# Performance work log

Measured on AMD Instinct MI355X. Metric: run time of the kernel, lower is better.

## Reference

```python
import jax, jax.numpy as jnp
import numpy as np
from jax import lax

B, NM, P, F, E, H, K = 32, 131072, 256, 3, 64, 4, 3
DH = E // H


def layer_norm(x, gamma, beta, eps=1e-5):
    mu = x.mean(-1, keepdims=True)
    var = ((x - mu) ** 2).mean(-1, keepdims=True)
    return (x - mu) * lax.rsqrt(var + eps) * gamma + beta


def knn_interp(x, pos_x, pos_y, k=K):
    """x: [B, Nx, F] features at pos_x [Nx, 2]; interpolate to pos_y [Ny, 2].
    Positions are shared across the batch (they are tiled in the torch code),
    so KNN indices/weights are computed once. Matches torch knn + inverse-
    squared-distance weighted scatter (uniform per-batch counts => gather form).
    """
    d2 = jnp.sum((pos_y[:, None, :] - pos_x[None, :, :]) ** 2, axis=-1)  # [Ny, Nx]
    neg_d2, idx = lax.top_k(-d2, k)                                      # [Ny, k]
    w = 1.0 / jnp.clip(-neg_d2, 1e-16)                                   # [Ny, k]
    w = lax.stop_gradient(w)  # torch computes weights under no_grad
    gathered = x[:, idx, :]                                              # [B, Ny, k, F]
    num = jnp.sum(gathered * w[None, :, :, None], axis=2)                # [B, Ny, F]
    den = jnp.sum(w, axis=1)[None, :, None]                              # [1, Ny, 1]
    return num / den


def setup_inputs() -> dict:
    key = jax.random.key(0)
    ks = jax.random.split(key, 8)
    return {
        "node_attr": jax.random.normal(ks[0], (B * NM, F), jnp.float32),
        "position_mesh": jax.random.uniform(ks[1], (NM, 2), jnp.float32),
        "position_pivotal": jax.random.uniform(ks[2], (P, 2), jnp.float32),
        "ln_gamma": jnp.ones((F,), jnp.float32),
        "ln_beta": jnp.zeros((F,), jnp.float32),
        "Wf": jax.random.normal(ks[3], (E, F), jnp.float32) * (2.0 / E) ** 0.5,
        "bf": jnp.zeros((E,), jnp.float32),
        "Wp": jax.random.normal(ks[4], (E, 2), jnp.float32) * (2.0 / E) ** 0.5,
        "bp": jnp.zeros((E,), jnp.float32),
        "in_proj_w": jax.random.normal(ks[5], (3 * E, E), jnp.float32) * (1.0 / E) ** 0.5,
        "in_proj_b": jnp.zeros((3 * E,), jnp.float32),
        "batch_size": B,
    }


def reference(node_attr, position_mesh, position_pivotal, ln_gamma, ln_beta,
              Wf, bf, Wp, bp, in_proj_w, in_proj_b, batch_size):
    x = node_attr.reshape(batch_size, -1, F)                 # [B, NM, F]
    # PivotalNorm after encoder (encoder/decoder MeshGraphNet omitted: undefined dep)
    x = layer_norm(x, ln_gamma, ln_beta)
    # ---- downsample: mesh -> pivotal via inverse-distance KNN interpolation ----
    y = knn_interp(x, position_mesh, position_pivotal)       # [B, P, F]
    # attention-based pooling over pivotal nodes
    q = (jnp.einsum('bpf,ef->bpe', y, Wf) + bf
         + (position_pivotal @ Wp.T + bp)[None])             # [B, P, E]
    Wq, Wk = in_proj_w[:E], in_proj_w[E:2 * E]
    bq, bk = in_proj_b[:E], in_proj_b[E:2 * E]
    Q = (q @ Wq.T + bq).reshape(batch_size, P, H, DH)
    Kt = (q @ Wk.T + bk).reshape(batch_size, P, H, DH)
    scores = jnp.einsum('bqhd,bkhd->bhqk', Q, Kt) / np.float32(np.sqrt(DH))
    attn = jax.nn.softmax(scores, axis=-1)                   # [B, H, P, P]
    attn_w = attn.mean(axis=1)                               # avg heads, [B, P, P]
    y = jnp.einsum('bqk,bkf->bqf', attn_w, y)                # [B, P, F]
    # ---- interpolate: pivotal -> mesh ----
    out = knn_interp(y, position_pivotal, position_mesh)     # [B, NM, F]
    return out.reshape(-1, F)
```

## Files before the change

kernel.cpp:

```cpp
#include <hip/hip_runtime.h>
#include <math.h>

#define NM 131072
#define PP 256
#define BB 32
#define INF_F 3.0e38f

#define GM   64
#define GM2  (GM * GM)
#define CAPM 96
#define GP   16
#define GP2  (GP * GP)
#define CAPP 8

typedef unsigned long long u64;

__device__ __forceinline__ u64 packkey(float d, int i) {
  return ((u64)__float_as_uint(d) << 32) | (unsigned)i;
}

__device__ __forceinline__ void ins3k(u64 k, u64& k0, u64& k1, u64& k2) {
  bool l0 = k < k0, l1 = k < k1, l2 = k < k2;
  k2 = l1 ? k1 : (l2 ? k : k2);
  k1 = l0 ? k0 : (l1 ? k : k1);
  k0 = l0 ? k : k0;
}

__device__ __forceinline__ float dist2(float ax, float ay, float bx, float by) {
  float dx = ax - bx, dy = ay - by;
  return __fadd_rn(__fmul_rn(dx, dx), __fmul_rn(dy, dy));
}

__global__ __launch_bounds__(256)
void build_buckets(const float* __restrict__ mesh, const float* __restrict__ piv,
                   unsigned* __restrict__ cntM, unsigned* __restrict__ cntP,
                   unsigned* __restrict__ ovfc,
                   float* __restrict__ bufM,
                   int* __restrict__ bufP,
                   float* __restrict__ ovfM, int* __restrict__ ovfP,
                   float* __restrict__ y2) {
  const int g = blockIdx.x * 256 + threadIdx.x;
  if (g < NM) {
    float2 mp = ((const float2*)mesh)[g];
    int cx = min((int)(mp.x * GM), GM - 1);
    int cy = min((int)(mp.y * GM), GM - 1);
    int c = cy * GM + cx;
    unsigned s = atomicAdd(&cntM[c], 1u);
    if (s < CAPM) {
      float* d = bufM + (size_t)(c * CAPM + s) * 3;
      d[0] = mp.x; d[1] = mp.y; ((int*)d)[2] = g;
    } else {
      unsigned o = atomicAdd(&ovfc[0], 1u);
      float* d = ovfM + (size_t)o * 3;
      d[0] = mp.x; d[1] = mp.y; ((int*)d)[2] = g;
    }
  }
  if (blockIdx.x == 0 && threadIdx.x < PP) {
    const int p = threadIdx.x;
    float2 pv = ((const float2*)piv)[p];
    int cx = min((int)(pv.x * GP), GP - 1);
    int cy = min((int)(pv.y * GP), GP - 1);
    int c = cy * GP + cx;
    unsigned s = atomicAdd(&cntP[c], 1u);
    if (s < CAPP) bufP[c * CAPP + s] = p;
    else { unsigned o = atomicAdd(&ovfc[1], 1u); ovfP[o] = p; }
  }
  if (blockIdx.x == 1) {
    for (int j = threadIdx.x; j < BB * PP * 4; j += 256) y2[j] = 0.f;
  }
}

__global__ __launch_bounds__(256)
void knnA_grid(const float* __restrict__ piv,
               const unsigned* __restrict__ cntM, const float* __restrict__ bufM,
               const unsigned* __restrict__ ovfc, const float* __restrict__ ovfM,
               float* __restrict__ wA, int* __restrict__ idxA) {
  const int p = blockIdx.x;
  const int t = threadIdx.x;
  __shared__ u64 sk[256 * 3];
  __shared__ u64 g3[3];
  __shared__ int sdone;

  const float2 pv = ((const float2*)piv)[p];
  const int cx = min((int)(pv.x * GM), GM - 1);
  const int cy = min((int)(pv.y * GM), GM - 1);

  u64 b0 = ~0ull, b1 = ~0ull, b2 = ~0ull;

  {
    int x0 = max(cx - 1, 0), x1 = min(cx + 1, GM - 1);
    int y0 = max(cy - 1, 0), y1 = min(cy + 1, GM - 1);
    for (int yy = y0; yy <= y1; ++yy) {
      int cb = yy * GM + x0;
      int tot = (x1 - x0 + 1) * CAPM;
      for (int s = t; s < tot; s += 256) {
        int ci = s / CAPM, j = s - ci * CAPM;
        int c = cb + ci;
        if (j < (int)min(cntM[c], (unsigned)CAPM)) {
          const float* cp = bufM + (size_t)(c * CAPM + j) * 3;
          float d = dist2(pv.x, pv.y, cp[0], cp[1]);
          ins3k(packkey(d, ((const int*)cp)[2]), b0, b1, b2);
        }
      }
    }
    int no = (int)ovfc[0];
    for (int j = t; j < no; j += 256) {
      const float* cp = ovfM + (size_t)j * 3;
      float d = dist2(pv.x, pv.y, cp[0], cp[1]);
      ins3k(packkey(d, ((const int*)cp)[2]), b0, b1, b2);
    }
  }

  int R = 1;
  u64 p0 = ~0ull, p1 = ~0ull, p2 = ~0ull;
  while (true) {
    sk[t * 3 + 0] = b0; sk[t * 3 + 1] = b1; sk[t * 3 + 2] = b2;
    __syncthreads();
    if (t < 32) {
      u64 e0 = ~0ull, e1 = ~0ull, e2 = ~0ull;
#pragma unroll
      for (int s = 0; s < 8; ++s) {
        int o = (t + 32 * s) * 3;
        ins3k(sk[o], e0, e1, e2); ins3k(sk[o + 1], e0, e1, e2); ins3k(sk[o + 2], e0, e1, e2);
      }
      sk[t * 3] = e0; sk[t * 3 + 1] = e1; sk[t * 3 + 2] = e2;
    }
    __syncthreads();
    if (t == 0) {
      u64 e0 = p0, e1 = p1, e2 = p2;
      for (int s = 0; s < 32; ++s) {
        ins3k(sk[s * 3], e0, e1, e2); ins3k(sk[s * 3 + 1], e0, e1, e2); ins3k(sk[s * 3 + 2], e0, e1, e2);
      }
      g3[0] = e0; g3[1] = e1; g3[2] = e2;
      float d2f = __uint_as_float((unsigned)(e2 >> 32));
      float md = (float)R * (1.0f / GM);
      sdone = (md * md > d2f) ? 1 : 0;
    }
    __syncthreads();
    if (sdone) break;
    p0 = g3[0]; p1 = g3[1]; p2 = g3[2];
    b0 = b1 = b2 = ~0ull;
    R += 1;
    int x0 = max(cx - R, 0), x1 = min(cx + R, GM - 1);
    for (int pass = 0; pass < 2; ++pass) {
      int yy = pass ? cy + R : cy - R;
      if (yy < 0 || yy > GM - 1) continue;
      int cb = yy * GM + x0;
      int tot = (x1 - x0 + 1) * CAPM;
      for (int s = t; s < tot; s += 256) {
        int ci = s / CAPM, j = s - ci * CAPM;
        int c = cb + ci;
        if (j < (int)min(cntM[c], (unsigned)CAPM)) {
          const float* cp = bufM + (size_t)(c * CAPM + j) * 3;
          float d = dist2(pv.x, pv.y, cp[0], cp[1]);
          ins3k(packkey(d, ((const int*)cp)[2]), b0, b1, b2);
        }
      }
    }
    int yy0 = max(cy - R + 1, 0), yy1 = min(cy + R - 1, GM - 1);
    for (int pass = 0; pass < 2; ++pass) {
      int xx = pass ? cx + R : cx - R;
      if (xx < 0 || xx > GM - 1) continue;
      int tot = (yy1 - yy0 + 1) * CAPM;
      for (int s = t; s < tot; s += 256) {
        int ri = s / CAPM, j = s - ri * CAPM;
        int c = (yy0 + ri) * GM + xx;
        if (j < (int)min(cntM[c], (unsigned)CAPM)) {
          const float* cp = bufM + (size_t)(c * CAPM + j) * 3;
          float d = dist2(pv.x, pv.y, cp[0], cp[1]);
          ins3k(packkey(d, ((const int*)cp)[2]), b0, b1, b2);
        }
      }
    }
    __syncthreads();
  }
  if (t == 0) {
#pragma unroll
    for (int k = 0; k < 3; ++k) {
      u64 e = g3[k];
      float d = __uint_as_float((unsigned)(e >> 32));
      wA[p * 3 + k] = 1.0f / fmaxf(d, 1e-16f);
      idxA[p * 3 + k] = (int)(unsigned)(e & 0xffffffffu);
    }
  }
}

__global__ __launch_bounds__(128, 2)
void gather_qqk(const float* __restrict__ node, const float* __restrict__ piv,
                const float* __restrict__ gamma, const float* __restrict__ beta,
                const float* __restrict__ Wf, const float* __restrict__ bf,
                const float* __restrict__ Wp, const float* __restrict__ bp,
                const float* __restrict__ ipw, const float* __restrict__ ipb,
                const float* __restrict__ wA, const int* __restrict__ idxA,
                float* __restrict__ y, float* __restrict__ Qh, float* __restrict__ Kh) {
  const int b = blockIdx.x >> 5;
  const int ptile = (blockIdx.x & 31) * 8;
  const int t = threadIdx.x;
  __shared__ float qs[8][64];
  __shared__ float ys[8][3];

  if (t < 8) {
    const int p = ptile + t;
    const float g0 = gamma[0], g1 = gamma[1], g2 = gamma[2];
    const float be0 = beta[0], be1 = beta[1], be2 = beta[2];
    float num0 = 0.f, num1 = 0.f, num2 = 0.f, den = 0.f;
#pragma unroll
    for (int k = 0; k < 3; ++k) {
      int idx = idxA[p * 3 + k];
      float w = wA[p * 3 + k];
      const float* r = node + ((size_t)b * NM + idx) * 3;
      float a0 = r[0], a1 = r[1], a2 = r[2];
      float mu = (a0 + a1 + a2) * (1.0f / 3.0f);
      float e0 = a0 - mu, e1 = a1 - mu, e2 = a2 - mu;
      float var = (e0 * e0 + e1 * e1 + e2 * e2) * (1.0f / 3.0f);
      float sc = 1.0f / sqrtf(var + 1e-5f);
      num0 += (e0 * sc * g0 + be0) * w;
      num1 += (e1 * sc * g1 + be1) * w;
      num2 += (e2 * sc * g2 + be2) * w;
      den += w;
    }
    float o0 = num0 / den, o1 = num1 / den, o2 = num2 / den;
    ys[t][0] = o0; ys[t][1] = o1; ys[t][2] = o2;
    float* yr = y + (b * PP + p) * 3;
    yr[0] = o0; yr[1] = o1; yr[2] = o2;
  }
  __syncthreads();

  const int e = t & 63;
  const int half = t >> 6;
  {
    float wf0 = Wf[e * 3], wf1 = Wf[e * 3 + 1], wf2 = Wf[e * 3 + 2];
    float wp0 = Wp[e * 2], wp1 = Wp[e * 2 + 1];
    float cst = bf[e] + bp[e];
    for (int r = half; r < 8; r += 2) {
      int p = ptile + r;
      float pe = piv[2 * p] * wp0 + piv[2 * p + 1] * wp1;
      qs[r][e] = ys[r][0] * wf0 + ys[r][1] * wf1 + ys[r][2] * wf2 + cst + pe;
    }
  }
  __syncthreads();

  const int row = half * 64 + e;
  float wreg[64];
  const float4* W4 = (const float4*)(ipw + row * 64);
#pragma unroll
  for (int j = 0; j < 16; ++j) {
    float4 v = W4[j];
    wreg[4 * j] = v.x; wreg[4 * j + 1] = v.y; wreg[4 * j + 2] = v.z; wreg[4 * j + 3] = v.w;
  }
  float bias = ipb[row];
  float* dst = half ? Kh : Qh;
  const int h = e >> 4, d = e & 15;
  for (int r = 0; r < 8; ++r) {
    float acc = bias;
#pragma unroll
    for (int j = 0; j < 64; ++j) acc += qs[r][j] * wreg[j];
    int p = ptile + r;
    dst[(((b * 4 + h) * PP) + p) * 16 + d] = acc;
  }
}

__global__ __launch_bounds__(256, 2)
void attn_kernel(const float* __restrict__ Qh, const float* __restrict__ Kh,
                 const float* __restrict__ y, float* __restrict__ y2) {
  const int b = blockIdx.x >> 4;
  const int h = (blockIdx.x >> 2) & 3;
  const int qq = blockIdx.x & 3;
  const int t = threadIdx.x;
  const int sub = t & 7;
  const int rt = t >> 3;

  __shared__ float4 sK[PP * 5];
  __shared__ float4 sY[PP];

  {
    const float4* src = (const float4*)(Kh + (size_t)(b * 4 + h) * PP * 16);
#pragma unroll
    for (int i = t; i < PP * 4; i += 256) {
      int k = i >> 2, j = i & 3;
      sK[k * 5 + j] = src[i];
    }
    const float* yr = y + (b * PP + t) * 3;
    sY[t] = make_float4(yr[0], yr[1], yr[2], 0.f);
  }
  __syncthreads();

  const int q0 = qq * 64 + rt * 2;
  const float4* q4 = (const float4*)(Qh + ((size_t)((b * 4 + h) * PP) + q0) * 16);
  float4 A0 = q4[0], A1 = q4[1], A2 = q4[2], A3 = q4[3];
  float4 B0 = q4[4], B1 = q4[5], B2 = q4[6], B3 = q4[7];

  float m0 = -INF_F, l0 = 0.f, x0 = 0.f, x1 = 0.f, x2 = 0.f;
  float m1 = -INF_F, l1 = 0.f, z0 = 0.f, z1 = 0.f, z2 = 0.f;

#pragma unroll 4
  for (int kk = 0; kk < 32; ++kk) {
    int k = kk * 8 + sub;
    float4 K0 = sK[k * 5 + 0], K1 = sK[k * 5 + 1], K2 = sK[k * 5 + 2], K3 = sK[k * 5 + 3];
    float4 yv = sY[k];
    float s0 = (A0.x*K0.x + A0.y*K0.y + A0.z*K0.z + A0.w*K0.w
              + A1.x*K1.x + A1.y*K1.y + A1.z*K1.z + A1.w*K1.w
              + A2.x*K2.x + A2.y*K2.y + A2.z*K2.z + A2.w*K2.w
              + A3.x*K3.x + A3.y*K3.y + A3.z*K3.z + A3.w*K3.w) * 0.25f;
    float s1 = (B0.x*K0.x + B0.y*K0.y + B0.z*K0.z + B0.w*K0.w
              + B1.x*K1.x + B1.y*K1.y + B1.z*K1.z + B1.w*K1.w
              + B2.x*K2.x + B2.y*K2.y + B2.z*K2.z + B2.w*K2.w
              + B3.x*K3.x + B3.y*K3.y + B3.z*K3.z + B3.w*K3.w) * 0.25f;
    {
      float mn = fmaxf(m0, s0);
      float p = __expf(s0 - mn), sc = __expf(m0 - mn);
      l0 = l0 * sc + p;
      x0 = x0 * sc + p * yv.x; x1 = x1 * sc + p * yv.y; x2 = x2 * sc + p * yv.z;
      m0 = mn;
    }
    {
      float mn = fmaxf(m1, s1);
      float p = __expf(s1 - mn), sc = __expf(m1 - mn);
      l1 = l1 * sc + p;
      z0 = z0 * sc + p * yv.x; z1 = z1 * sc + p * yv.y; z2 = z2 * sc + p * yv.z;
      m1 = mn;
    }
  }

#pragma unroll
  for (int off = 1; off < 8; off <<= 1) {
    float mo = __shfl_xor(m0, off), lo = __shfl_xor(l0, off);
    float b0 = __shfl_xor(x0, off), b1 = __shfl_xor(x1, off), b2 = __shfl_xor(x2, off);
    float M = fmaxf(m0, mo);
    float es = __expf(m0 - M), eo = __expf(mo - M);
    l0 = l0 * es + lo * eo;
    x0 = x0 * es + b0 * eo; x1 = x1 * es + b1 * eo; x2 = x2 * es + b2 * eo;
    m0 = M;

    float mo1 = __shfl_xor(m1, off), lo1 = __shfl_xor(l1, off);
    float c0 = __shfl_xor(z0, off), c1 = __shfl_xor(z1, off), c2 = __shfl_xor(z2, off);
    float M1 = fmaxf(m1, mo1);
    float es1 = __expf(m1 - M1), eo1 = __expf(mo1 - M1);
    l1 = l1 * es1 + lo1 * eo1;
    z0 = z0 * es1 + c0 * eo1; z1 = z1 * es1 + c1 * eo1; z2 = z2 * es1 + c2 * eo1;
    m1 = M1;
  }

  if (sub == 0) {
    float inv0 = 0.25f / l0;
    float inv1 = 0.25f / l1;
    float* o0 = y2 + (size_t)(b * PP + q0) * 4;
    atomicAdd(o0 + 0, x0 * inv0);
    atomicAdd(o0 + 1, x1 * inv0);
    atomicAdd(o0 + 2, x2 * inv0);
    float* o1 = o0 + 4;
    atomicAdd(o1 + 0, z0 * inv1);
    atomicAdd(o1 + 1, z1 * inv1);
    atomicAdd(o1 + 2, z2 * inv1);
  }
}

__global__ __launch_bounds__(256)
void knnB_search(const float* __restrict__ mesh, const float* __restrict__ piv,
                 const unsigned* __restrict__ cntP, const int* __restrict__ bufP,
                 const unsigned* __restrict__ ovfc, const int* __restrict__ ovfP,
                 float4* __restrict__ wB4, int4* __restrict__ idxB4) {
  const int t = threadIdx.x;
  __shared__ float spx[PP], spy[PP];
  __shared__ unsigned scnt[GP2];
  __shared__ int sbuf[GP2 * CAPP];
  {
    float2 pvv = ((const float2*)piv)[t];
    spx[t] = pvv.x; spy[t] = pvv.y;
    scnt[t] = cntP[t];
    for (int j = t; j < GP2 * CAPP; j += 256) sbuf[j] = bufP[j];
  }
  __syncthreads();

  const int m = blockIdx.x * 256 + t;
  const float2 mv = ((const float2*)mesh)[m];
  const int cx = min((int)(mv.x * GP), GP - 1);
  const int cy = min((int)(mv.y * GP), GP - 1);
  u64 k0 = ~0ull, k1 = ~0ull, k2 = ~0ull;

  {
    int x0 = max(cx - 2, 0), x1 = min(cx + 2, GP - 1);
    int y0 = max(cy - 2, 0), y1 = min(cy + 2, GP - 1);
    for (int yy = y0; yy <= y1; ++yy)
      for (int xx = x0; xx <= x1; ++xx) {
        int c = yy * GP + xx;
        int n = (int)min(scnt[c], (unsigned)CAPP);
        for (int j = 0; j < n; ++j) {
          int qq = sbuf[c * CAPP + j];
          float d = dist2(mv.x, mv.y, spx[qq], spy[qq]);
          ins3k(packkey(d, qq), k0, k1, k2);
        }
      }
    int no = (int)ovfc[1];
    for (int j = 0; j < no; ++j) {
      int qq = ovfP[j];
      float d = dist2(mv.x, mv.y, spx[qq], spy[qq]);
      ins3k(packkey(d, qq), k0, k1, k2);
    }
  }
  int R = 2;
  while (true) {
    float d2f = __uint_as_float((unsigned)(k2 >> 32));
    float md = (float)R * (1.0f / GP);
    if (md * md > d2f) break;
    R += 1;
    if (R >= 2 * GP) break;
    int x0 = max(cx - R, 0), x1 = min(cx + R, GP - 1);
    for (int pass = 0; pass < 2; ++pass) {
      int yy = pass ? cy + R : cy - R;
      if (yy < 0 || yy > GP - 1) continue;
      for (int xx = x0; xx <= x1; ++xx) {
        int c = yy * GP + xx;
        int n = (int)min(scnt[c], (unsigned)CAPP);
        for (int j = 0; j < n; ++j) {
          int qq = sbuf[c * CAPP + j];
          float d = dist2(mv.x, mv.y, spx[qq], spy[qq]);
          ins3k(packkey(d, qq), k0, k1, k2);
        }
      }
    }
    int yy0 = max(cy - R + 1, 0), yy1 = min(cy + R - 1, GP - 1);
    for (int pass = 0; pass < 2; ++pass) {
      int xx = pass ? cx + R : cx - R;
      if (xx < 0 || xx > GP - 1) continue;
      for (int yy = yy0; yy <= yy1; ++yy) {
        int c = yy * GP + xx;
        int n = (int)min(scnt[c], (unsigned)CAPP);
        for (int j = 0; j < n; ++j) {
          int qq = sbuf[c * CAPP + j];
          float d = dist2(mv.x, mv.y, spx[qq], spy[qq]);
          ins3k(packkey(d, qq), k0, k1, k2);
        }
      }
    }
  }

  float d0 = __uint_as_float((unsigned)(k0 >> 32));
  float d1 = __uint_as_float((unsigned)(k1 >> 32));
  float d2v = __uint_as_float((unsigned)(k2 >> 32));
  float w0 = 1.0f / fmaxf(d0, 1e-16f);
  float w1 = 1.0f / fmaxf(d1, 1e-16f);
  float w2 = 1.0f / fmaxf(d2v, 1e-16f);
  float inv = 1.0f / (w0 + w1 + w2);
  wB4[m] = make_float4(w0, w1, w2, inv);
  idxB4[m] = make_int4((int)(unsigned)(k0 & 0xffffffffu),
                       (int)(unsigned)(k1 & 0xffffffffu),
                       (int)(unsigned)(k2 & 0xffffffffu), 0);
}

__global__ __launch_bounds__(256)
void interp_out(const float4* __restrict__ y2, const float4* __restrict__ wB4,
                const int4* __restrict__ idxB4, float* __restrict__ out) {
  const int t = threadIdx.x;
  const int mt = blockIdx.x >> 2;
  const int bg = blockIdx.x & 3;
  __shared__ float4 sy[8 * PP];
  {
    const float4* src = y2 + bg * 8 * PP;
#pragma unroll
    for (int j = 0; j < 8; ++j) sy[t + 256 * j] = src[t + 256 * j];
  }
  __syncthreads();

  const int m = mt * 256 + t;
  const float4 w = wB4[m];
  const int4 ix = idxB4[m];

#pragma unroll
  for (int i = 0; i < 8; ++i) {
    const float4* yb = sy + i * PP;
    float4 r0 = yb[ix.x];
    float4 r1 = yb[ix.y];
    float4 r2 = yb[ix.z];
    float3 res;
    res.x = (w.x * r0.x + w.y * r1.x + w.z * r2.x) * w.w;
    res.y = (w.x * r0.y + w.y * r1.y + w.z * r2.y) * w.w;
    res.z = (w.x * r0.z + w.y * r1.z + w.z * r2.z) * w.w;
    const int b = bg * 8 + i;
    *(float3*)(out + ((size_t)b * NM + m) * 3) = res;
  }
}

extern "C" void kernel_launch(void* const* d_in, const int* in_sizes, int n_in,
                              void* d_out, int out_size, void* d_ws, size_t ws_size,
                              hipStream_t stream) {
  const float* node  = (const float*)d_in[0];
  const float* mesh  = (const float*)d_in[1];
  const float* piv   = (const float*)d_in[2];
  const float* gamma = (const float*)d_in[3];
  const float* beta  = (const float*)d_in[4];
  const float* Wf    = (const float*)d_in[5];
  const float* bf    = (const float*)d_in[6];
  const float* Wp    = (const float*)d_in[7];
  const float* bp    = (const float*)d_in[8];
  const float* ipw   = (const float*)d_in[9];
  const float* ipb   = (const float*)d_in[10];
  float* out = (float*)d_out;

  unsigned* cntM = (unsigned*)d_ws;
  unsigned* cntP = cntM + 4096;
  unsigned* ovfc = cntP + 256;
  float* bufM = (float*)d_ws + 4608;
  int*   bufP = (int*)(bufM + (size_t)GM2 * CAPM * 3);
  float* ovfM = (float*)(bufP + GP2 * CAPP);
  int*   ovfP = (int*)(ovfM + (size_t)NM * 3);
  float* wA   = (float*)(ovfP + PP);
  int*   idxA = (int*)(wA + PP * 3);
  float* y    = (float*)(idxA + PP * 3);
  float* Qh   = y + BB * PP * 3;
  float* Kh   = Qh + BB * PP * 64;
  float* y2   = Kh + BB * PP * 64;
  float4* wB4   = (float4*)(y2 + BB * PP * 4);
  int4*   idxB4 = (int4*)(wB4 + NM);

  hipMemsetAsync(cntM, 0, 4608 * sizeof(unsigned), stream);
  build_buckets<<<NM / 256, 256, 0, stream>>>(mesh, piv, cntM, cntP, ovfc,
                                              bufM, bufP, ovfM, ovfP, y2);
  knnA_grid<<<PP, 256, 0, stream>>>(piv, cntM, bufM, ovfc, ovfM, wA, idxA);
  knnB_search<<<NM / 256, 256, 0, stream>>>(mesh, piv, cntP, bufP, ovfc, ovfP, wB4, idxB4);
  gather_qqk<<<BB * 32, 128, 0, stream>>>(node, piv, gamma, beta, Wf, bf, Wp, bp, ipw, ipb,
                                          wA, idxA, y, Qh, Kh);
  attn_kernel<<<BB * 4 * 4, 256, 0, stream>>>(Qh, Kh, y, y2);
  interp_out<<<NM / 256 * 4, 256, 0, stream>>>((const float4*)y2, wB4, idxB4, out);
}
```

Before: 195.0 us.

## Fuse all six stages into one cooperative persistent kernel with grid syncs

```diff
diff --git a/kernel.cpp b/kernel.cpp
--- a/kernel.cpp
+++ b/kernel.cpp
@@ -1,5 +1,8 @@
 #include <hip/hip_runtime.h>
+#include <hip/hip_cooperative_groups.h>
 #include <math.h>
+
+namespace cg = cooperative_groups;
 
 #define NM 131072
 #define PP 256
@@ -31,16 +34,54 @@
   return __fadd_rn(__fmul_rn(dx, dx), __fmul_rn(dy, dy));
 }
 
-__global__ __launch_bounds__(256)
-void build_buckets(const float* __restrict__ mesh, const float* __restrict__ piv,
-                   unsigned* __restrict__ cntM, unsigned* __restrict__ cntP,
-                   unsigned* __restrict__ ovfc,
-                   float* __restrict__ bufM,
-                   int* __restrict__ bufP,
-                   float* __restrict__ ovfM, int* __restrict__ ovfP,
-                   float* __restrict__ y2) {
-  const int g = blockIdx.x * 256 + threadIdx.x;
-  if (g < NM) {
+union SMem {
+  struct { u64 sk[PP * 3]; u64 g3[3]; int sdone; } a;
+  struct { float spx[PP], spy[PP]; unsigned scnt[GP2]; int sbuf[GP2 * CAPP]; } b;
+  struct { float qs[2][8][64]; float ys[2][8][3]; } g;
+  struct { float4 sK[PP * 5]; float4 sY[PP]; } at;
+  struct { float4 sy[8 * PP]; } ip;
+};
+
+__global__ __launch_bounds__(256, 2)
+void mega(const float* __restrict__ node, const float* __restrict__ mesh,
+          const float* __restrict__ piv, const float* __restrict__ gamma,
+          const float* __restrict__ beta, const float* __restrict__ Wf,
+          const float* __restrict__ bf, const float* __restrict__ Wp,
+          const float* __restrict__ bp, const float* __restrict__ ipw,
+          const float* __restrict__ ipb, float* __restrict__ out,
+          float* __restrict__ ws) {
+  cg::grid_group grid = cg::this_grid();
+  const int blk = blockIdx.x;
+  const int t = threadIdx.x;
+  __shared__ SMem sm;
+
+  unsigned* cntM = (unsigned*)ws;
+  unsigned* cntP = cntM + 4096;
+  unsigned* ovfc = cntP + 256;
+  float* bufM = ws + 4608;
+  int*   bufP = (int*)(bufM + (size_t)GM2 * CAPM * 3);
+  float* ovfM = (float*)(bufP + GP2 * CAPP);
+  int*   ovfP = (int*)(ovfM + (size_t)NM * 3);
+  float* wA   = (float*)(ovfP + PP);
+  int*   idxA = (int*)(wA + PP * 3);
+  float* y    = (float*)(idxA + PP * 3);
+  float* Qh   = y + BB * PP * 3;
+  float* Kh   = Qh + BB * PP * 64;
+  float* y2   = Kh + BB * PP * 64;
+  float4* wB4   = (float4*)(y2 + BB * PP * 4);
+  int4*   idxB4 = (int4*)(wB4 + NM);
+
+  {
+    const int idx = blk * 256 + t;
+    if (idx < BB * PP * 4) y2[idx] = 0.f;
+    if (idx < 4096) cntM[idx] = 0u;
+    if (idx < GP2) cntP[idx] = 0u;
+    if (idx < 2) ovfc[idx] = 0u;
+  }
+  grid.sync();
+
+  {
+    const int g = blk * 256 + t;
     float2 mp = ((const float2*)mesh)[g];
     int cx = min((int)(mp.x * GM), GM - 1);
     int cy = min((int)(mp.y * GM), GM - 1);
@@ -54,430 +95,398 @@
       float* d = ovfM + (size_t)o * 3;
       d[0] = mp.x; d[1] = mp.y; ((int*)d)[2] = g;
     }
+    if (blk == 0) {
+      const int p = t;
+      float2 pv = ((const float2*)piv)[p];
+      int px = min((int)(pv.x * GP), GP - 1);
+      int py = min((int)(pv.y * GP), GP - 1);
+      int pc = py * GP + px;
+      unsigned ps = atomicAdd(&cntP[pc], 1u);
+      if (ps < CAPP) bufP[pc * CAPP + ps] = p;
+      else { unsigned o = atomicAdd(&ovfc[1], 1u); ovfP[o] = p; }
+    }
   }
-  if (blockIdx.x == 0 && threadIdx.x < PP) {
-    const int p = threadIdx.x;
-    float2 pv = ((const float2*)piv)[p];
-    int cx = min((int)(pv.x * GP), GP - 1);
-    int cy = min((int)(pv.y * GP), GP - 1);
-    int c = cy * GP + cx;
-    unsigned s = atomicAdd(&cntP[c], 1u);
-    if (s < CAPP) bufP[c * CAPP + s] = p;
-    else { unsigned o = atomicAdd(&ovfc[1], 1u); ovfP[o] = p; }
+  grid.sync();
+
+  if (blk < 256) {
+    const int p = blk;
+    const float2 pv = ((const float2*)piv)[p];
+    const int cx = min((int)(pv.x * GM), GM - 1);
+    const int cy = min((int)(pv.y * GM), GM - 1);
+
+    u64 b0 = ~0ull, b1 = ~0ull, b2 = ~0ull;
+    {
+      int x0 = max(cx - 1, 0), x1 = min(cx + 1, GM - 1);
+      int y0 = max(cy - 1, 0), y1 = min(cy + 1, GM - 1);
+      for (int yy = y0; yy <= y1; ++yy) {
+        int cb = yy * GM + x0;
+        int tot = (x1 - x0 + 1) * CAPM;
+        for (int s = t; s < tot; s += 256) {
+          int ci = s / CAPM, j = s - ci * CAPM;
+          int c = cb + ci;
+          if (j < (int)min(cntM[c], (unsigned)CAPM)) {
+            const float* cp = bufM + (size_t)(c * CAPM + j) * 3;
+            float d = dist2(pv.x, pv.y, cp[0], cp[1]);
+            ins3k(packkey(d, ((const int*)cp)[2]), b0, b1, b2);
+          }
+        }
+      }
+      int no = (int)ovfc[0];
+      for (int j = t; j < no; j += 256) {
+        const float* cp = ovfM + (size_t)j * 3;
+        float d = dist2(pv.x, pv.y, cp[0], cp[1]);
+        ins3k(packkey(d, ((const int*)cp)[2]), b0, b1, b2);
+      }
+    }
+
+    int R = 1;
+    u64 p0 = ~0ull, p1 = ~0ull, p2 = ~0ull;
+    while (true) {
+      sm.a.sk[t * 3 + 0] = b0; sm.a.sk[t * 3 + 1] = b1; sm.a.sk[t * 3 + 2] = b2;
+      __syncthreads();
+      if (t < 32) {
+        u64 e0 = ~0ull, e1 = ~0ull, e2 = ~0ull;
+#pragma unroll
+        for (int s = 0; s < 8; ++s) {
+          int o = (t + 32 * s) * 3;
+          ins3k(sm.a.sk[o], e0, e1, e2); ins3k(sm.a.sk[o + 1], e0, e1, e2); ins3k(sm.a.sk[o + 2], e0, e1, e2);
+        }
+        sm.a.sk[t * 3] = e0; sm.a.sk[t * 3 + 1] = e1; sm.a.sk[t * 3 + 2] = e2;
+      }
+      __syncthreads();
+      if (t == 0) {
+        u64 e0 = p0, e1 = p1, e2 = p2;
+        for (int s = 0; s < 32; ++s) {
+          ins3k(sm.a.sk[s * 3], e0, e1, e2); ins3k(sm.a.sk[s * 3 + 1], e0, e1, e2); ins3k(sm.a.sk[s * 3 + 2], e0, e1, e2);
+        }
+        sm.a.g3[0] = e0; sm.a.g3[1] = e1; sm.a.g3[2] = e2;
+        float d2f = __uint_as_float((unsigned)(e2 >> 32));
+        float md = (float)R * (1.0f / GM);
+        sm.a.sdone = (md * md > d2f) ? 1 : 0;
+      }
+      __syncthreads();
+      if (sm.a.sdone) break;
+      p0 = sm.a.g3[0]; p1 = sm.a.g3[1]; p2 = sm.a.g3[2];
+      b0 = b1 = b2 = ~0ull;
+      R += 1;
+      int x0 = max(cx - R, 0), x1 = min(cx + R, GM - 1);
+      for (int pass = 0; pass < 2; ++pass) {
+        int yy = pass ? cy + R : cy - R;
+        if (yy < 0 || yy > GM - 1) continue;
+        int cb = yy * GM + x0;
+        int tot = (x1 - x0 + 1) * CAPM;
+        for (int s = t; s < tot; s += 256) {
+          int ci = s / CAPM, j = s - ci * CAPM;
+          int c = cb + ci;
+          if (j < (int)min(cntM[c], (unsigned)CAPM)) {
+            const float* cp = bufM + (size_t)(c * CAPM + j) * 3;
+            float d = dist2(pv.x, pv.y, cp[0], cp[1]);
+            ins3k(packkey(d, ((const int*)cp)[2]), b0, b1, b2);
+          }
+        }
+      }
+      int yy0 = max(cy - R + 1, 0), yy1 = min(cy + R - 1, GM - 1);
+      for (int pass = 0; pass < 2; ++pass) {
+        int xx = pass ? cx + R : cx - R;
+        if (xx < 0 || xx > GM - 1) continue;
+        int tot = (yy1 - yy0 + 1) * CAPM;
+        for (int s = t; s < tot; s += 256) {
+          int ri = s / CAPM, j = s - ri * CAPM;
+          int c = (yy0 + ri) * GM + xx;
+          if (j < (int)min(cntM[c], (unsigned)CAPM)) {
+            const float* cp = bufM + (size_t)(c * CAPM + j) * 3;
+            float d = dist2(pv.x, pv.y, cp[0], cp[1]);
+            ins3k(packkey(d, ((const int*)cp)[2]), b0, b1, b2);
+          }
+        }
+      }
+      __syncthreads();
+    }
+    if (t == 0) {
+#pragma unroll
+      for (int k = 0; k < 3; ++k) {
+        u64 e = sm.a.g3[k];
+        float d = __uint_as_float((unsigned)(e >> 32));
+        wA[p * 3 + k] = 1.0f / fmaxf(d, 1e-16f);
+        idxA[p * 3 + k] = (int)(unsigned)(e & 0xffffffffu);
+      }
+    }
+  } else {
+    {
+      float2 pvv = ((const float2*)piv)[t];
+      sm.b.spx[t] = pvv.x; sm.b.spy[t] = pvv.y;
+      sm.b.scnt[t] = cntP[t];
+      for (int j = t; j < GP2 * CAPP; j += 256) sm.b.sbuf[j] = bufP[j];
+    }
+    __syncthreads();
+
+    for (int rep = 0; rep < 2; ++rep) {
+      const int m = (blk - 256 + rep * 256) * 256 + t;
+      const float2 mv = ((const float2*)mesh)[m];
+      const int cx = min((int)(mv.x * GP), GP - 1);
+      const int cy = min((int)(mv.y * GP), GP - 1);
+      u64 k0 = ~0ull, k1 = ~0ull, k2 = ~0ull;
+
+      {
+        int x0 = max(cx - 2, 0), x1 = min(cx + 2, GP - 1);
+        int y0 = max(cy - 2, 0), y1 = min(cy + 2, GP - 1);
+        for (int yy = y0; yy <= y1; ++yy)
+          for (int xx = x0; xx <= x1; ++xx) {
+            int c = yy * GP + xx;
+            int n = (int)min(sm.b.scnt[c], (unsigned)CAPP);
+            for (int j = 0; j < n; ++j) {
+              int qq = sm.b.sbuf[c * CAPP + j];
+              float d = dist2(mv.x, mv.y, sm.b.spx[qq], sm.b.spy[qq]);
+              ins3k(packkey(d, qq), k0, k1, k2);
+            }
+          }
+        int no = (int)ovfc[1];
+        for (int j = 0; j < no; ++j) {
+          int qq = ovfP[j];
+          float d = dist2(mv.x, mv.y, sm.b.spx[qq], sm.b.spy[qq]);
+          ins3k(packkey(d, qq), k0, k1, k2);
+        }
+      }
+      int R = 2;
+      while (true) {
+        float d2f = __uint_as_float((unsigned)(k2 >> 32));
+        float md = (float)R * (1.0f / GP);
+        if (md * md > d2f) break;
+        R += 1;
+        if (R >= 2 * GP) break;
+        int x0 = max(cx - R, 0), x1 = min(cx + R, GP - 1);
+        for (int pass = 0; pass < 2; ++pass) {
+          int yy = pass ? cy + R : cy - R;
+          if (yy < 0 || yy > GP - 1) continue;
+          for (int xx = x0; xx <= x1; ++xx) {
+            int c = yy * GP + xx;
+            int n = (int)min(sm.b.scnt[c], (unsigned)CAPP);
+            for (int j = 0; j < n; ++j) {
+              int qq = sm.b.sbuf[c * CAPP + j];
+              float d = dist2(mv.x, mv.y, sm.b.spx[qq], sm.b.spy[qq]);
+              ins3k(packkey(d, qq), k0, k1, k2);
+            }
+          }
+        }
+        int yy0 = max(cy - R + 1, 0), yy1 = min(cy + R - 1, GP - 1);
+        for (int pass = 0; pass < 2; ++pass) {
+          int xx = pass ? cx + R : cx - R;
+          if (xx < 0 || xx > GP - 1) continue;
+          for (int yy = yy0; yy <= yy1; ++yy) {
+            int c = yy * GP + xx;
+            int n = (int)min(sm.b.scnt[c], (unsigned)CAPP);
+            for (int j = 0; j < n; ++j) {
+              int qq = sm.b.sbuf[c * CAPP + j];
+              float d = dist2(mv.x, mv.y, sm.b.spx[qq], sm.b.spy[qq]);
+              ins3k(packkey(d, qq), k0, k1, k2);
+            }
+          }
+        }
+      }
+
+      float d0 = __uint_as_float((unsigned)(k0 >> 32));
+      float d1 = __uint_as_float((unsigned)(k1 >> 32));
+      float d2v = __uint_as_float((unsigned)(k2 >> 32));
+      float w0 = 1.0f / fmaxf(d0, 1e-16f);
+      float w1 = 1.0f / fmaxf(d1, 1e-16f);
+      float w2 = 1.0f / fmaxf(d2v, 1e-16f);
+      float inv = 1.0f / (w0 + w1 + w2);
+      wB4[m] = make_float4(w0, w1, w2, inv);
+      idxB4[m] = make_int4((int)(unsigned)(k0 & 0xffffffffu),
+                           (int)(unsigned)(k1 & 0xffffffffu),
+                           (int)(unsigned)(k2 & 0xffffffffu), 0);
+    }
   }
-  if (blockIdx.x == 1) {
-    for (int j = threadIdx.x; j < BB * PP * 4; j += 256) y2[j] = 0.f;
+  grid.sync();
+
+  {
+    const int hi = t >> 7, tl = t & 127;
+    const int ob = 2 * blk + hi;
+    const int b = ob >> 5;
+    const int ptile = (ob & 31) * 8;
+    float (*qs)[64] = sm.g.qs[hi];
+    float (*ys)[3] = sm.g.ys[hi];
+
+    if (tl < 8) {
+      const int p = ptile + tl;
+      const float g0 = gamma[0], g1 = gamma[1], g2 = gamma[2];
+      const float be0 = beta[0], be1 = beta[1], be2 = beta[2];
+      float num0 = 0.f, num1 = 0.f, num2 = 0.f, den = 0.f;
+#pragma unroll
+      for (int k = 0; k < 3; ++k) {
+        int idx = idxA[p * 3 + k];
+        float w = wA[p * 3 + k];
+        const float* r = node + ((size_t)b * NM + idx) * 3;
+        float a0 = r[0], a1 = r[1], a2 = r[2];
+        float mu = (a0 + a1 + a2) * (1.0f / 3.0f);
+        float e0 = a0 - mu, e1 = a1 - mu, e2 = a2 - mu;
+        float var = (e0 * e0 + e1 * e1 + e2 * e2) * (1.0f / 3.0f);
+        float sc = 1.0f / sqrtf(var + 1e-5f);
+        num0 += (e0 * sc * g0 + be0) * w;
+        num1 += (e1 * sc * g1 + be1) * w;
+        num2 += (e2 * sc * g2 + be2) * w;
+        den += w;
+      }
+      float o0 = num0 / den, o1 = num1 / den, o2 = num2 / den;
+      ys[tl][0] = o0; ys[tl][1] = o1; ys[tl][2] = o2;
+      float* yr = y + (b * PP + p) * 3;
+      yr[0] = o0; yr[1] = o1; yr[2] = o2;
+    }
+    __syncthreads();
+
+    const int e = tl & 63;
+    const int half = tl >> 6;
+    {
+      float wf0 = Wf[e * 3], wf1 = Wf[e * 3 + 1], wf2 = Wf[e * 3 + 2];
+      float wp0 = Wp[e * 2], wp1 = Wp[e * 2 + 1];
+      float cst = bf[e] + bp[e];
+      for (int r = half; r < 8; r += 2) {
+        int p = ptile + r;
+        float pe = piv[2 * p] * wp0 + piv[2 * p + 1] * wp1;
+        qs[r][e] = ys[r][0] * wf0 + ys[r][1] * wf1 + ys[r][2] * wf2 + cst + pe;
+      }
+    }
+    __syncthreads();
+
+    const int row = half * 64 + e;
+    float wreg[64];
+    const float4* W4 = (const float4*)(ipw + row * 64);
+#pragma unroll
+    for (int j = 0; j < 16; ++j) {
+      float4 v = W4[j];
+      wreg[4 * j] = v.x; wreg[4 * j + 1] = v.y; wreg[4 * j + 2] = v.z; wreg[4 * j + 3] = v.w;
+    }
+    float bias = ipb[row];
+    float* dst = half ? Kh : Qh;
+    const int h = e >> 4, d = e & 15;
+    for (int r = 0; r < 8; ++r) {
+      float acc = bias;
+#pragma unroll
+      for (int j = 0; j < 64; ++j) acc += qs[r][j] * wreg[j];
+      int p = ptile + r;
+      dst[(((b * 4 + h) * PP) + p) * 16 + d] = acc;
+    }
   }
-}
-
-__global__ __launch_bounds__(256)
-void knnA_grid(const float* __restrict__ piv,
-               const unsigned* __restrict__ cntM, const float* __restrict__ bufM,
-               const unsigned* __restrict__ ovfc, const float* __restrict__ ovfM,
-               float* __restrict__ wA, int* __restrict__ idxA) {
-  const int p = blockIdx.x;
-  const int t = threadIdx.x;
-  __shared__ u64 sk[256 * 3];
-  __shared__ u64 g3[3];
-  __shared__ int sdone;
-
-  const float2 pv = ((const float2*)piv)[p];
-  const int cx = min((int)(pv.x * GM), GM - 1);
-  const int cy = min((int)(pv.y * GM), GM - 1);
-
-  u64 b0 = ~0ull, b1 = ~0ull, b2 = ~0ull;
+  grid.sync();
 
   {
-    int x0 = max(cx - 1, 0), x1 = min(cx + 1, GM - 1);
-    int y0 = max(cy - 1, 0), y1 = min(cy + 1, GM - 1);
-    for (int yy = y0; yy <= y1; ++yy) {
-      int cb = yy * GM + x0;
-      int tot = (x1 - x0 + 1) * CAPM;
-      for (int s = t; s < tot; s += 256) {
-        int ci = s / CAPM, j = s - ci * CAPM;
-        int c = cb + ci;
-        if (j < (int)min(cntM[c], (unsigned)CAPM)) {
-          const float* cp = bufM + (size_t)(c * CAPM + j) * 3;
-          float d = dist2(pv.x, pv.y, cp[0], cp[1]);
-          ins3k(packkey(d, ((const int*)cp)[2]), b0, b1, b2);
-        }
-      }
-    }
-    int no = (int)ovfc[0];
-    for (int j = t; j < no; j += 256) {
-      const float* cp = ovfM + (size_t)j * 3;
-      float d = dist2(pv.x, pv.y, cp[0], cp[1]);
-      ins3k(packkey(d, ((const int*)cp)[2]), b0, b1, b2);
+    const int b = blk >> 4;
+    const int h = (blk >> 2) & 3;
+    const int qq = blk & 3;
+    const int sub = t & 7;
+    const int rt = t >> 3;
+
+    {
+      const float4* src = (const float4*)(Kh + (size_t)(b * 4 + h) * PP * 16);
+#pragma unroll
+      for (int i = t; i < PP * 4; i += 256) {
+        int k = i >> 2, j = i & 3;
+        sm.at.sK[k * 5 + j] = src[i];
+      }
+      const float* yr = y + (b * PP + t) * 3;
+      sm.at.sY[t] = make_float4(yr[0], yr[1], yr[2], 0.f);
+    }
+    __syncthreads();
+
+    const int q0 = qq * 64 + rt * 2;
+    const float4* q4 = (const float4*)(Qh + ((size_t)((b * 4 + h) * PP) + q0) * 16);
+    float4 A0 = q4[0], A1 = q4[1], A2 = q4[2], A3 = q4[3];
+    float4 B0 = q4[4], B1 = q4[5], B2 = q4[6], B3 = q4[7];
+
+    float m0 = -INF_F, l0 = 0.f, x0 = 0.f, x1 = 0.f, x2 = 0.f;
+    float m1 = -INF_F, l1 = 0.f, z0 = 0.f, z1 = 0.f, z2 = 0.f;
+
+#pragma unroll 4
+    for (int kk = 0; kk < 32; ++kk) {
+      int k = kk * 8 + sub;
+      float4 K0 = sm.at.sK[k * 5 + 0], K1 = sm.at.sK[k * 5 + 1];
+      float4 K2 = sm.at.sK[k * 5 + 2], K3 = sm.at.sK[k * 5 + 3];
+      float4 yv = sm.at.sY[k];
+      float s0 = (A0.x*K0.x + A0.y*K0.y + A0.z*K0.z + A0.w*K0.w
+                + A1.x*K1.x + A1.y*K1.y + A1.z*K1.z + A1.w*K1.w
+                + A2.x*K2.x + A2.y*K2.y + A2.z*K2.z + A2.w*K2.w
+                + A3.x*K3.x + A3.y*K3.y + A3.z*K3.z + A3.w*K3.w) * 0.25f;
+      float s1 = (B0.x*K0.x + B0.y*K0.y + B0.z*K0.z + B0.w*K0.w
+                + B1.x*K1.x + B1.y*K1.y + B1.z*K1.z + B1.w*K1.w
+                + B2.x*K2.x + B2.y*K2.y + B2.z*K2.z + B2.w*K2.w
+                + B3.x*K3.x + B3.y*K3.y + B3.z*K3.z + B3.w*K3.w) * 0.25f;
+      {
+        float mn = fmaxf(m0, s0);
+        float p = __expf(s0 - mn), sc = __expf(m0 - mn);
+        l0 = l0 * sc + p;
+        x0 = x0 * sc + p * yv.x; x1 = x1 * sc + p * yv.y; x2 = x2 * sc + p * yv.z;
+        m0 = mn;
+      }
+      {
+        float mn = fmaxf(m1, s1);
+        float p = __expf(s1 - mn), sc = __expf(m1 - mn);
+        l1 = l1 * sc + p;
+        z0 = z0 * sc + p * yv.x; z1 = z1 * sc + p * yv.y; z2 = z2 * sc + p * yv.z;
+        m1 = mn;
+      }
+    }
+
+#pragma unroll
+    for (int off = 1; off < 8; off <<= 1) {
+      float mo = __shfl_xor(m0, off), lo = __shfl_xor(l0, off);
+      float c0 = __shfl_xor(x0, off), c1 = __shfl_xor(x1, off), c2 = __shfl_xor(x2, off);
+      float M = fmaxf(m0, mo);
+      float es = __expf(m0 - M), eo = __expf(mo - M);
+      l0 = l0 * es + lo * eo;
+      x0 = x0 * es + c0 * eo; x1 = x1 * es + c1 * eo; x2 = x2 * es + c2 * eo;
+      m0 = M;
+
+      float mo1 = __shfl_xor(m1, off), lo1 = __shfl_xor(l1, off);
+      float e0 = __shfl_xor(z0, off), e1 = __shfl_xor(z1, off), e2 = __shfl_xor(z2, off);
+      float M1 = fmaxf(m1, mo1);
+      float es1 = __expf(m1 - M1), eo1 = __expf(mo1 - M1);
+      l1 = l1 * es1 + lo1 * eo1;
+      z0 = z0 * es1 + e0 * eo1; z1 = z1 * es1 + e1 * eo1; z2 = z2 * es1 + e2 * eo1;
+      m1 = M1;
+    }
+
+    if (sub == 0) {
+      float inv0 = 0.25f / l0;
+      float inv1 = 0.25f / l1;
+      float* o0 = y2 + (size_t)(b * PP + q0) * 4;
+      atomicAdd(o0 + 0, x0 * inv0);
+      atomicAdd(o0 + 1, x1 * inv0);
+      atomicAdd(o0 + 2, x2 * inv0);
+      float* o1 = o0 + 4;
+      atomicAdd(o1 + 0, z0 * inv1);
+      atomicAdd(o1 + 1, z1 * inv1);
+      atomicAdd(o1 + 2, z2 * inv1);
     }
   }
-
-  int R = 1;
-  u64 p0 = ~0ull, p1 = ~0ull, p2 = ~0ull;
-  while (true) {
-    sk[t * 3 + 0] = b0; sk[t * 3 + 1] = b1; sk[t * 3 + 2] = b2;
-    __syncthreads();
-    if (t < 32) {
-      u64 e0 = ~0ull, e1 = ~0ull, e2 = ~0ull;
-#pragma unroll
-      for (int s = 0; s < 8; ++s) {
-        int o = (t + 32 * s) * 3;
-        ins3k(sk[o], e0, e1, e2); ins3k(sk[o + 1], e0, e1, e2); ins3k(sk[o + 2], e0, e1, e2);
-      }
-      sk[t * 3] = e0; sk[t * 3 + 1] = e1; sk[t * 3 + 2] = e2;
-    }
-    __syncthreads();
-    if (t == 0) {
-      u64 e0 = p0, e1 = p1, e2 = p2;
-      for (int s = 0; s < 32; ++s) {
-        ins3k(sk[s * 3], e0, e1, e2); ins3k(sk[s * 3 + 1], e0, e1, e2); ins3k(sk[s * 3 + 2], e0, e1, e2);
-      }
-      g3[0] = e0; g3[1] = e1; g3[2] = e2;
-      float d2f = __uint_as_float((unsigned)(e2 >> 32));
-      float md = (float)R * (1.0f / GM);
-      sdone = (md * md > d2f) ? 1 : 0;
-    }
-    __syncthreads();
-    if (sdone) break;
-    p0 = g3[0]; p1 = g3[1]; p2 = g3[2];
-    b0 = b1 = b2 = ~0ull;
-    R += 1;
-    int x0 = max(cx - R, 0), x1 = min(cx + R, GM - 1);
-    for (int pass = 0; pass < 2; ++pass) {
-      int yy = pass ? cy + R : cy - R;
-      if (yy < 0 || yy > GM - 1) continue;
-      int cb = yy * GM + x0;
-      int tot = (x1 - x0 + 1) * CAPM;
-      for (int s = t; s < tot; s += 256) {
-        int ci = s / CAPM, j = s - ci * CAPM;
-        int c = cb + ci;
-        if (j < (int)min(cntM[c], (unsigned)CAPM)) {
-          const float* cp = bufM + (size_t)(c * CAPM + j) * 3;
-          float d = dist2(pv.x, pv.y, cp[0], cp[1]);
-          ins3k(packkey(d, ((const int*)cp)[2]), b0, b1, b2);
-        }
-      }
-    }
-    int yy0 = max(cy - R + 1, 0), yy1 = min(cy + R - 1, GM - 1);
-    for (int pass = 0; pass < 2; ++pass) {
-      int xx = pass ? cx + R : cx - R;
-      if (xx < 0 || xx > GM - 1) continue;
-      int tot = (yy1 - yy0 + 1) * CAPM;
-      for (int s = t; s < tot; s += 256) {
-        int ri = s / CAPM, j = s - ri * CAPM;
-        int c = (yy0 + ri) * GM + xx;
-        if (j < (int)min(cntM[c], (unsigned)CAPM)) {
-          const float* cp = bufM + (size_t)(c * CAPM + j) * 3;
-          float d = dist2(pv.x, pv.y, cp[0], cp[1]);
-          ins3k(packkey(d, ((const int*)cp)[2]), b0, b1, b2);
-        }
-      }
-    }
-    __syncthreads();
-  }
-  if (t == 0) {
-#pragma unroll
-    for (int k = 0; k < 3; ++k) {
-      u64 e = g3[k];
-      float d = __uint_as_float((unsigned)(e >> 32));
-      wA[p * 3 + k] = 1.0f / fmaxf(d, 1e-16f);
-      idxA[p * 3 + k] = (int)(unsigned)(e & 0xffffffffu);
-    }
-  }
-}
-
-__global__ __launch_bounds__(128, 2)
-void gather_qqk(const float* __restrict__ node, const float* __restrict__ piv,
-                const float* __restrict__ gamma, const float* __restrict__ beta,
-                const float* __restrict__ Wf, const float* __restrict__ bf,
-                const float* __restrict__ Wp, const float* __restrict__ bp,
-                const float* __restrict__ ipw, const float* __restrict__ ipb,
-                const float* __restrict__ wA, const int* __restrict__ idxA,
-                float* __restrict__ y, float* __restrict__ Qh, float* __restrict__ Kh) {
-  const int b = blockIdx.x >> 5;
-  const int ptile = (blockIdx.x & 31) * 8;
-  const int t = threadIdx.x;
-  __shared__ float qs[8][64];
-  __shared__ float ys[8][3];
-
-  if (t < 8) {
-    const int p = ptile + t;
-    const float g0 = gamma[0], g1 = gamma[1], g2 = gamma[2];
-    const float be0 = beta[0], be1 = beta[1], be2 = beta[2];
-    float num0 = 0.f, num1 = 0.f, num2 = 0.f, den = 0.f;
-#pragma unroll
-    for (int k = 0; k < 3; ++k) {
-      int idx = idxA[p * 3 + k];
-      float w = wA[p * 3 + k];
-      const float* r = node + ((size_t)b * NM + idx) * 3;
-      float a0 = r[0], a1 = r[1], a2 = r[2];
-      float mu = (a0 + a1 + a2) * (1.0f / 3.0f);
-      float e0 = a0 - mu, e1 = a1 - mu, e2 = a2 - mu;
-      float var = (e0 * e0 + e1 * e1 + e2 * e2) * (1.0f / 3.0f);
-      float sc = 1.0f / sqrtf(var + 1e-5f);
-      num0 += (e0 * sc * g0 + be0) * w;
-      num1 += (e1 * sc * g1 + be1) * w;
-      num2 += (e2 * sc * g2 + be2) * w;
-      den += w;
-    }
-    float o0 = num0 / den, o1 = num1 / den, o2 = num2 / den;
-    ys[t][0] = o0; ys[t][1] = o1; ys[t][2] = o2;
-    float* yr = y + (b * PP + p) * 3;
-    yr[0] = o0; yr[1] = o1; yr[2] = o2;
-  }
-  __syncthreads();
-
-  const int e = t & 63;
-  const int half = t >> 6;
+  grid.sync();
+
   {
-    float wf0 = Wf[e * 3], wf1 = Wf[e * 3 + 1], wf2 = Wf[e * 3 + 2];
-    float wp0 = Wp[e * 2], wp1 = Wp[e * 2 + 1];
-    float cst = bf[e] + bp[e];
-    for (int r = half; r < 8; r += 2) {
-      int p = ptile + r;
-      float pe = piv[2 * p] * wp0 + piv[2 * p + 1] * wp1;
-      qs[r][e] = ys[r][0] * wf0 + ys[r][1] * wf1 + ys[r][2] * wf2 + cst + pe;
-    }
-  }
-  __syncthreads();
-
-  const int row = half * 64 + e;
-  float wreg[64];
-  const float4* W4 = (const float4*)(ipw + row * 64);
-#pragma unroll
-  for (int j = 0; j < 16; ++j) {
-    float4 v = W4[j];
-    wreg[4 * j] = v.x; wreg[4 * j + 1] = v.y; wreg[4 * j + 2] = v.z; wreg[4 * j + 3] = v.w;
-  }
-  float bias = ipb[row];
-  float* dst = half ? Kh : Qh;
-  const int h = e >> 4, d = e & 15;
-  for (int r = 0; r < 8; ++r) {
-    float acc = bias;
-#pragma unroll
-    for (int j = 0; j < 64; ++j) acc += qs[r][j] * wreg[j];
-    int p = ptile + r;
-    dst[(((b * 4 + h) * PP) + p) * 16 + d] = acc;
-  }
-}
-
-__global__ __launch_bounds__(256, 2)
-void attn_kernel(const float* __restrict__ Qh, const float* __restrict__ Kh,
-                 const float* __restrict__ y, float* __restrict__ y2) {
-  const int b = blockIdx.x >> 4;
-  const int h = (blockIdx.x >> 2) & 3;
-  const int qq = blockIdx.x & 3;
-  const int t = threadIdx.x;
-  const int sub = t & 7;
-  const int rt = t >> 3;
-
-  __shared__ float4 sK[PP * 5];
-  __shared__ float4 sY[PP];
-
-  {
-    const float4* src = (const float4*)(Kh + (size_t)(b * 4 + h) * PP * 16);
-#pragma unroll
-    for (int i = t; i < PP * 4; i += 256) {
-      int k = i >> 2, j = i & 3;
-      sK[k * 5 + j] = src[i];
-    }
-    const float* yr = y + (b * PP + t) * 3;
-    sY[t] = make_float4(yr[0], yr[1], yr[2], 0.f);
-  }
-  __syncthreads();
-
-  const int q0 = qq * 64 + rt * 2;
-  const float4* q4 = (const float4*)(Qh + ((size_t)((b * 4 + h) * PP) + q0) * 16);
-  float4 A0 = q4[0], A1 = q4[1], A2 = q4[2], A3 = q4[3];
-  float4 B0 = q4[4], B1 = q4[5], B2 = q4[6], B3 = q4[7];
-
-  float m0 = -INF_F, l0 = 0.f, x0 = 0.f, x1 = 0.f, x2 = 0.f;
-  float m1 = -INF_F, l1 = 0.f, z0 = 0.f, z1 = 0.f, z2 = 0.f;
-
-#pragma unroll 4
-  for (int kk = 0; kk < 32; ++kk) {
-    int k = kk * 8 + sub;
-    float4 K0 = sK[k * 5 + 0], K1 = sK[k * 5 + 1], K2 = sK[k * 5 + 2], K3 = sK[k * 5 + 3];
-    float4 yv = sY[k];
-    float s0 = (A0.x*K0.x + A0.y*K0.y + A0.z*K0.z + A0.w*K0.w
-              + A1.x*K1.x + A1.y*K1.y + A1.z*K1.z + A1.w*K1.w
-              + A2.x*K2.x + A2.y*K2.y + A2.z*K2.z + A2.w*K2.w
-              + A3.x*K3.x + A3.y*K3.y + A3.z*K3.z + A3.w*K3.w) * 0.25f;
-    float s1 = (B0.x*K0.x + B0.y*K0.y + B0.z*K0.z + B0.w*K0.w
-              + B1.x*K1.x + B1.y*K1.y + B1.z*K1.z + B1.w*K1.w
-              + B2.x*K2.x + B2.y*K2.y + B2.z*K2.z + B2.w*K2.w
-              + B3.x*K3.x + B3.y*K3.y + B3.z*K3.z + B3.w*K3.w) * 0.25f;
-    {
-      float mn = fmaxf(m0, s0);
-      float p = __expf(s0 - mn), sc = __expf(m0 - mn);
-      l0 = l0 * sc + p;
-      x0 = x0 * sc + p * yv.x; x1 = x1 * sc + p * yv.y; x2 = x2 * sc + p * yv.z;
-      m0 = mn;
-    }
-    {
-      float mn = fmaxf(m1, s1);
-      float p = __expf(s1 - mn), sc = __expf(m1 - mn);
-      l1 = l1 * sc + p;
-      z0 = z0 * sc + p * yv.x; z1 = z1 * sc + p * yv.y; z2 = z2 * sc + p * yv.z;
-      m1 = mn;
-    }
-  }
-
-#pragma unroll
-  for (int off = 1; off < 8; off <<= 1) {
-    float mo = __shfl_xor(m0, off), lo = __shfl_xor(l0, off);
-    float b0 = __shfl_xor(x0, off), b1 = __shfl_xor(x1, off), b2 = __shfl_xor(x2, off);
-    float M = fmaxf(m0, mo);
-    float es = __expf(m0 - M), eo = __expf(mo - M);
-    l0 = l0 * es + lo * eo;
-    x0 = x0 * es + b0 * eo; x1 = x1 * es + b1 * eo; x2 = x2 * es + b2 * eo;
-    m0 = M;
-
-    float mo1 = __shfl_xor(m1, off), lo1 = __shfl_xor(l1, off);
-    float c0 = __shfl_xor(z0, off), c1 = __shfl_xor(z1, off), c2 = __shfl_xor(z2, off);
-    float M1 = fmaxf(m1, mo1);
-    float es1 = __expf(m1 - M1), eo1 = __expf(mo1 - M1);
-    l1 = l1 * es1 + lo1 * eo1;
-    z0 = z0 * es1 + c0 * eo1; z1 = z1 * es1 + c1 * eo1; z2 = z2 * es1 + c2 * eo1;
-    m1 = M1;
-  }
-
-  if (sub == 0) {
-    float inv0 = 0.25f / l0;
-    float inv1 = 0.25f / l1;
-    float* o0 = y2 + (size_t)(b * PP + q0) * 4;
-    atomicAdd(o0 + 0, x0 * inv0);
-    atomicAdd(o0 + 1, x1 * inv0);
-    atomicAdd(o0 + 2, x2 * inv0);
-    float* o1 = o0 + 4;
-    atomicAdd(o1 + 0, z0 * inv1);
-    atomicAdd(o1 + 1, z1 * inv1);
-    atomicAdd(o1 + 2, z2 * inv1);
-  }
-}
-
-__global__ __launch_bounds__(256)
-void knnB_search(const float* __restrict__ mesh, const float* __restrict__ piv,
-                 const unsigned* __restrict__ cntP, const int* __restrict__ bufP,
-                 const unsigned* __restrict__ ovfc, const int* __restrict__ ovfP,
-                 float4* __restrict__ wB4, int4* __restrict__ idxB4) {
-  const int t = threadIdx.x;
-  __shared__ float spx[PP], spy[PP];
-  __shared__ unsigned scnt[GP2];
-  __shared__ int sbuf[GP2 * CAPP];
-  {
-    float2 pvv = ((const float2*)piv)[t];
-    spx[t] = pvv.x; spy[t] = pvv.y;
-    scnt[t] = cntP[t];
-    for (int j = t; j < GP2 * CAPP; j += 256) sbuf[j] = bufP[j];
-  }
-  __syncthreads();
-
-  const int m = blockIdx.x * 256 + t;
-  const float2 mv = ((const float2*)mesh)[m];
-  const int cx = min((int)(mv.x * GP), GP - 1);
-  const int cy = min((int)(mv.y * GP), GP - 1);
-  u64 k0 = ~0ull, k1 = ~0ull, k2 = ~0ull;
-
-  {
-    int x0 = max(cx - 2, 0), x1 = min(cx + 2, GP - 1);
-    int y0 = max(cy - 2, 0), y1 = min(cy + 2, GP - 1);
-    for (int yy = y0; yy <= y1; ++yy)
-      for (int xx = x0; xx <= x1; ++xx) {
-        int c = yy * GP + xx;
-        int n = (int)min(scnt[c], (unsigned)CAPP);
-        for (int j = 0; j < n; ++j) {
-          int qq = sbuf[c * CAPP + j];
-          float d = dist2(mv.x, mv.y, spx[qq], spy[qq]);
-          ins3k(packkey(d, qq), k0, k1, k2);
-        }
-      }
-    int no = (int)ovfc[1];
-    for (int j = 0; j < no; ++j) {
-      int qq = ovfP[j];
-      float d = dist2(mv.x, mv.y, spx[qq], spy[qq]);
-      ins3k(packkey(d, qq), k0, k1, k2);
-    }
-  }
-  int R = 2;
-  while (true) {
-    float d2f = __uint_as_float((unsigned)(k2 >> 32));
-    float md = (float)R * (1.0f / GP);
-    if (md * md > d2f) break;
-    R += 1;
-    if (R >= 2 * GP) break;
-    int x0 = max(cx - R, 0), x1 = min(cx + R, GP - 1);
-    for (int pass = 0; pass < 2; ++pass) {
-      int yy = pass ? cy + R : cy - R;
-      if (yy < 0 || yy > GP - 1) continue;
-      for (int xx = x0; xx <= x1; ++xx) {
-        int c = yy * GP + xx;
-        int n = (int)min(scnt[c], (unsigned)CAPP);
-        for (int j = 0; j < n; ++j) {
-          int qq = sbuf[c * CAPP + j];
-          float d = dist2(mv.x, mv.y, spx[qq], spy[qq]);
-          ins3k(packkey(d, qq), k0, k1, k2);
-        }
-      }
-    }
-    int yy0 = max(cy - R + 1, 0), yy1 = min(cy + R - 1, GP - 1);
-    for (int pass = 0; pass < 2; ++pass) {
-      int xx = pass ? cx + R : cx - R;
-      if (xx < 0 || xx > GP - 1) continue;
-      for (int yy = yy0; yy <= yy1; ++yy) {
-        int c = yy * GP + xx;
-        int n = (int)min(scnt[c], (unsigned)CAPP);
-        for (int j = 0; j < n; ++j) {
-          int qq = sbuf[c * CAPP + j];
-          float d = dist2(mv.x, mv.y, spx[qq], spy[qq]);
-          ins3k(packkey(d, qq), k0, k1, k2);
-        }
-      }
-    }
-  }
-
-  float d0 = __uint_as_float((unsigned)(k0 >> 32));
-  float d1 = __uint_as_float((unsigned)(k1 >> 32));
-  float d2v = __uint_as_float((unsigned)(k2 >> 32));
-  float w0 = 1.0f / fmaxf(d0, 1e-16f);
-  float w1 = 1.0f / fmaxf(d1, 1e-16f);
-  float w2 = 1.0f / fmaxf(d2v, 1e-16f);
-  float inv = 1.0f / (w0 + w1 + w2);
-  wB4[m] = make_float4(w0, w1, w2, inv);
-  idxB4[m] = make_int4((int)(unsigned)(k0 & 0xffffffffu),
-                       (int)(unsigned)(k1 & 0xffffffffu),
-                       (int)(unsigned)(k2 & 0xffffffffu), 0);
-}
-
-__global__ __launch_bounds__(256)
-void interp_out(const float4* __restrict__ y2, const float4* __restrict__ wB4,
-                const int4* __restrict__ idxB4, float* __restrict__ out) {
-  const int t = threadIdx.x;
-  const int mt = blockIdx.x >> 2;
-  const int bg = blockIdx.x & 3;
-  __shared__ float4 sy[8 * PP];
-  {
-    const float4* src = y2 + bg * 8 * PP;
-#pragma unroll
-    for (int j = 0; j < 8; ++j) sy[t + 256 * j] = src[t + 256 * j];
-  }
-  __syncthreads();
-
-  const int m = mt * 256 + t;
-  const float4 w = wB4[m];
-  const int4 ix = idxB4[m];
-
-#pragma unroll
-  for (int i = 0; i < 8; ++i) {
-    const float4* yb = sy + i * PP;
-    float4 r0 = yb[ix.x];
-    float4 r1 = yb[ix.y];
-    float4 r2 = yb[ix.z];
-    float3 res;
-    res.x = (w.x * r0.x + w.y * r1.x + w.z * r2.x) * w.w;
-    res.y = (w.x * r0.y + w.y * r1.y + w.z * r2.y) * w.w;
-    res.z = (w.x * r0.z + w.y * r1.z + w.z * r2.z) * w.w;
-    const int b = bg * 8 + i;
-    *(float3*)(out + ((size_t)b * NM + m) * 3) = res;
+    const int m = blk * 256 + t;
+    const float4 w = wB4[m];
+    const int4 ix = idxB4[m];
+    const float4* y4 = (const float4*)y2;
+
+    for (int bg = 0; bg < 4; ++bg) {
+      __syncthreads();
+      const float4* src = y4 + bg * 8 * PP;
+#pragma unroll
+      for (int j = 0; j < 8; ++j) sm.ip.sy[t + 256 * j] = src[t + 256 * j];
+      __syncthreads();
+
+#pragma unroll
+      for (int i = 0; i < 8; ++i) {
+        const float4* yb = sm.ip.sy + i * PP;
+        float4 r0 = yb[ix.x];
+        float4 r1 = yb[ix.y];
+        float4 r2 = yb[ix.z];
+        float3 res;
+        res.x = (w.x * r0.x + w.y * r1.x + w.z * r2.x) * w.w;
+        res.y = (w.x * r0.y + w.y * r1.y + w.z * r2.y) * w.w;
+        res.z = (w.x * r0.z + w.y * r1.z + w.z * r2.z) * w.w;
+        const int b = bg * 8 + i;
+        *(float3*)(out + ((size_t)b * NM + m) * 3) = res;
+      }
+    }
   }
 }
 
@@ -496,30 +505,12 @@
   const float* ipw   = (const float*)d_in[9];
   const float* ipb   = (const float*)d_in[10];
   float* out = (float*)d_out;
-
-  unsigned* cntM = (unsigned*)d_ws;
-  unsigned* cntP = cntM + 4096;
-  unsigned* ovfc = cntP + 256;
-  float* bufM = (float*)d_ws + 4608;
-  int*   bufP = (int*)(bufM + (size_t)GM2 * CAPM * 3);
-  float* ovfM = (float*)(bufP + GP2 * CAPP);
-  int*   ovfP = (int*)(ovfM + (size_t)NM * 3);
-  float* wA   = (float*)(ovfP + PP);
-  int*   idxA = (int*)(wA + PP * 3);
-  float* y    = (float*)(idxA + PP * 3);
-  float* Qh   = y + BB * PP * 3;
-  float* Kh   = Qh + BB * PP * 64;
-  float* y2   = Kh + BB * PP * 64;
-  float4* wB4   = (float4*)(y2 + BB * PP * 4);
-  int4*   idxB4 = (int4*)(wB4 + NM);
-
-  hipMemsetAsync(cntM, 0, 4608 * sizeof(unsigned), stream);
-  build_buckets<<<NM / 256, 256, 0, stream>>>(mesh, piv, cntM, cntP, ovfc,
-                                              bufM, bufP, ovfM, ovfP, y2);
-  knnA_grid<<<PP, 256, 0, stream>>>(piv, cntM, bufM, ovfc, ovfM, wA, idxA);
-  knnB_search<<<NM / 256, 256, 0, stream>>>(mesh, piv, cntP, bufP, ovfc, ovfP, wB4, idxB4);
-  gather_qqk<<<BB * 32, 128, 0, stream>>>(node, piv, gamma, beta, Wf, bf, Wp, bp, ipw, ipb,
-                                          wA, idxA, y, Qh, Kh);
-  attn_kernel<<<BB * 4 * 4, 256, 0, stream>>>(Qh, Kh, y, y2);
-  interp_out<<<NM / 256 * 4, 256, 0, stream>>>((const float4*)y2, wB4, idxB4, out);
+  float* ws = (float*)d_ws;
+
+  void* args[] = {
+    (void*)&node, (void*)&mesh, (void*)&piv, (void*)&gamma, (void*)&beta,
+    (void*)&Wf, (void*)&bf, (void*)&Wp, (void*)&bp, (void*)&ipw, (void*)&ipb,
+    (void*)&out, (void*)&ws
+  };
+  hipLaunchCooperativeKernel((void*)mega, dim3(512), dim3(256), args, 0, stream);
 }
```

Result: slower. 470.3 us (+141.1%).
